# Performance work log

Hardware: AMD Instinct MI355X
Metric: run time of the kernel (lower is better)

The kernel has to match this reference:

```python
import jax, jax.numpy as jnp
import numpy as np

N_NODES = 50000
N_EDGES = 800000
DIM = 128
LN_EPS = 1e-5


def setup_inputs() -> dict:
    key = jax.random.key(0)
    k1, k2, k3, k4 = jax.random.split(key, 4)
    h = jax.random.normal(k1, (N_NODES, DIM), dtype=jnp.float32)
    edge_index = jax.random.randint(k2, (2, N_EDGES), 0, N_NODES, dtype=jnp.int64)
    W = jax.random.normal(k3, (DIM, DIM), dtype=jnp.float32) / np.sqrt(DIM)
    b = jnp.zeros((DIM,), dtype=jnp.float32)
    gamma = jnp.ones((DIM,), dtype=jnp.float32)
    beta = jnp.zeros((DIM,), dtype=jnp.float32)
    t = jnp.zeros((), dtype=jnp.float32)
    return {"t": t, "h": h, "edge_index": edge_index, "batch_size": N_NODES,
            "W": W, "b": b, "gamma": gamma, "beta": beta}


def _gcn_conv(h, edge_index, W, b):
    """PyG-style GCNConv: D^{-1/2} (A+I) D^{-1/2} (h W) + b."""
    N = h.shape[0]
    loops = jnp.arange(N, dtype=edge_index.dtype)
    src = jnp.concatenate([edge_index[0], loops])  # [E+N]
    dst = jnp.concatenate([edge_index[1], loops])  # [E+N]
    # degree (with self loops) on destination nodes
    deg = jax.ops.segment_sum(jnp.ones_like(dst, dtype=h.dtype), dst, num_segments=N)
    dinv = jnp.where(deg > 0, jax.lax.rsqrt(deg), 0.0)
    norm = dinv[src] * dinv[dst]                    # [E+N]
    xw = h @ W                                      # [N, D]
    msg = xw[src] * norm[:, None]                   # gather + scale, [E+N, D]
    agg = jax.ops.segment_sum(msg, dst, num_segments=N)  # scatter-add, [N, D]
    return agg + b


def reference(t, h, edge_index, batch_size, W, b, gamma, beta):
    if h.ndim == 1:
        h = h[None, :]
    dh = _gcn_conv(h, edge_index, W, b)
    # LayerNorm over feature dim, then tanh
    mean = jnp.mean(dh, axis=-1, keepdims=True)
    var = jnp.mean(jnp.square(dh - mean), axis=-1, keepdims=True)
    dh = (dh - mean) * jax.lax.rsqrt(var + LN_EPS) * gamma + beta
    dh = jnp.tanh(dh)
    return (dh, jnp.zeros_like(edge_index), jnp.zeros_like(jnp.asarray(batch_size)))
```

## Files before the change

### kernel.cpp

```cpp
#include <hip/hip_runtime.h>
#include <math.h>

#define NN 50000
#define NE 800000
#define D  128
#define SCAN_CHUNK 1024
#define NSCAN ((NN + SCAN_CHUNK - 1) / SCAN_CHUNK)
#define PG_BLOCKS 782

typedef __attribute__((ext_vector_type(8))) short bf16x8;
typedef __attribute__((ext_vector_type(4))) float f32x4;

__device__ __forceinline__ unsigned short f32_to_bf16(float f) {
    unsigned u = __float_as_uint(f);
    u = u + 0x7FFFu + ((u >> 16) & 1u);
    return (unsigned short)(u >> 16);
}

__global__ __launch_bounds__(256) void k_count(
        const float* __restrict__ Wg, const int* __restrict__ ei,
        int* __restrict__ deg, unsigned short* __restrict__ rank,
        unsigned short* __restrict__ wpk, unsigned short* __restrict__ zb,
        int* __restrict__ outtail, int tailN) {
    int tid = threadIdx.x;
    int g = blockIdx.x * 256 + tid;

    if (g < NE / 4) {
        int4 d4 = ((const int4*)(ei + NE))[g];
        ushort4 r;
        r.x = (unsigned short)atomicAdd(&deg[d4.x], 1);
        r.y = (unsigned short)atomicAdd(&deg[d4.y], 1);
        r.z = (unsigned short)atomicAdd(&deg[d4.z], 1);
        r.w = (unsigned short)atomicAdd(&deg[d4.w], 1);
        ((ushort4*)rank)[g] = r;
    }
    for (int i = g; i < tailN; i += PG_BLOCKS * 256) outtail[i] = 0;

    if (blockIdx.x == 0) {
#pragma unroll 8
        for (int i = 0; i < 64; i++) {
            int o = i * 256 + tid;
            int j = o & 7, frag = o >> 3;
            int lo = frag & 15, quad = (frag >> 4) & 3;
            int kt = (frag >> 6) & 3, nt = frag >> 8;
            int k = kt * 32 + quad * 8 + j, n = nt * 16 + lo;
            wpk[o] = f32_to_bf16(Wg[k * 128 + n]);
        }
    }
    if (blockIdx.x == 1 && tid < 64)
        ((unsigned*)(zb + (size_t)NN * D))[tid] = 0u;
}

__global__ __launch_bounds__(256) void k_scan(const int* __restrict__ deg,
                                              int* __restrict__ partial,
                                              int* __restrict__ flag,
                                              int* __restrict__ rowoff,
                                              float* __restrict__ dinv) {
    __shared__ int sbuf[256];
    int t = threadIdx.x;
    int bid = blockIdx.x;
    int base = bid * SCAN_CHUNK + t * 4;
    int d[4]; int s = 0;
#pragma unroll
    for (int j = 0; j < 4; j++) {
        int i = base + j;
        d[j] = 0;
        if (i < NN) {
            d[j] = deg[i];
            s += d[j];
            dinv[i] = rsqrtf((float)d[j] + 1.0f);
        }
    }
    sbuf[t] = s; __syncthreads();
    for (int off = 1; off < 256; off <<= 1) {
        int v = (t >= off) ? sbuf[t - off] : 0;
        __syncthreads();
        sbuf[t] += v;
        __syncthreads();
    }
    if (t == 0) {
        atomicExch(&partial[bid], sbuf[255]);
        __threadfence();
        atomicAdd(flag, 1);
        while (atomicAdd(flag, 0) < NSCAN) {}
    }
    __syncthreads();

    int lane = t & 63;
    int pv = (lane < NSCAN && lane < bid) ? atomicAdd(&partial[lane], 0) : 0;
#pragma unroll
    for (int off = 32; off > 0; off >>= 1) pv += __shfl_xor(pv, off, 64);

    int ex = sbuf[t] - s + pv;
#pragma unroll
    for (int j = 0; j < 4; j++) {
        int i = base + j;
        if (i < NN) {
            rowoff[i] = ex;
            ex += d[j];
            if (i == NN - 1) rowoff[NN] = ex;
        }
    }
}

__global__ __launch_bounds__(256) void k_gemm_fill(
        const float* __restrict__ h, const uint4* __restrict__ wpk4,
        const int* __restrict__ ei, const unsigned short* __restrict__ rank,
        const int* __restrict__ rowoff, const float* __restrict__ dinv,
        unsigned short* __restrict__ zb, int* __restrict__ csr) {
    int tid = threadIdx.x;
    int g = blockIdx.x * 256 + tid;

    if (g < NE / 4) {
        int4 s4 = ((const int4*)ei)[g];
        int4 d4 = ((const int4*)(ei + NE))[g];
        ushort4 r4 = ((const ushort4*)rank)[g];
        csr[rowoff[d4.x] + r4.x] = s4.x;
        csr[rowoff[d4.y] + r4.y] = s4.y;
        csr[rowoff[d4.z] + r4.z] = s4.z;
        csr[rowoff[d4.w] + r4.w] = s4.w;
    }

    int w = tid >> 6, lane = tid & 63;
    int quad = lane >> 4, lo = lane & 15;
    int rowBase = blockIdx.x * 64 + w * 16;
    int rowA = rowBase + lo; if (rowA > NN - 1) rowA = NN - 1;
    const float4* h4 = (const float4*)h;

    bf16x8 af[4];
#pragma unroll
    for (int kt = 0; kt < 4; kt++) {
        float4 u = h4[(size_t)rowA * 32 + kt * 8 + quad * 2];
        float4 v = h4[(size_t)rowA * 32 + kt * 8 + quad * 2 + 1];
        bf16x8 a;
        a[0] = (short)f32_to_bf16(u.x); a[1] = (short)f32_to_bf16(u.y);
        a[2] = (short)f32_to_bf16(u.z); a[3] = (short)f32_to_bf16(u.w);
        a[4] = (short)f32_to_bf16(v.x); a[5] = (short)f32_to_bf16(v.y);
        a[6] = (short)f32_to_bf16(v.z); a[7] = (short)f32_to_bf16(v.w);
        af[kt] = a;
    }

    f32x4 acc[8];
#pragma unroll
    for (int nt = 0; nt < 8; nt++) acc[nt] = (f32x4){0.f, 0.f, 0.f, 0.f};

#pragma unroll
    for (int kt = 0; kt < 4; kt++) {
#pragma unroll
        for (int nt = 0; nt < 8; nt++) {
            uint4 tb = wpk4[nt * 256 + kt * 64 + lane];
            bf16x8 bfv = __builtin_bit_cast(bf16x8, tb);
            acc[nt] = __builtin_amdgcn_mfma_f32_16x16x32_bf16(af[kt], bfv, acc[nt], 0, 0, 0);
        }
    }

#pragma unroll
    for (int reg = 0; reg < 4; reg++) {
        int row = rowBase + quad * 4 + reg;
        if (row < NN) {
            float dn = dinv[row];
#pragma unroll
            for (int nt = 0; nt < 8; nt++)
                zb[(size_t)row * D + nt * 16 + lo] = f32_to_bf16(acc[nt][reg] * dn);
        }
    }
}

__global__ __launch_bounds__(256) void k_gather_ln(
        const int* __restrict__ rowoff, const int* __restrict__ csr,
        const float* __restrict__ dinv, const unsigned* __restrict__ zbu,
        const float* __restrict__ bias, const float* __restrict__ gamma,
        const float* __restrict__ beta, float* __restrict__ out) {
    int tid = threadIdx.x;
    int w = tid >> 6, lane = tid & 63;
    int rowBase = blockIdx.x * 16 + w * 4;

    float2 x[4];
#pragma unroll
    for (int r = 0; r < 4; r++) {
        int row = __builtin_amdgcn_readfirstlane(rowBase + r);
        float dn = dinv[row];
        unsigned zr = zbu[(size_t)row * 64 + lane];
        float2 a;
        a.x = __uint_as_float(zr << 16);
        a.y = __uint_as_float(zr & 0xFFFF0000u);
        int cs = __builtin_amdgcn_readfirstlane(rowoff[row]);
        int ce = __builtin_amdgcn_readfirstlane(rowoff[row + 1]);
        for (int c = cs; c < ce; c += 8) {
            int m = ce - c;
            int s[8];
#pragma unroll
            for (int q = 0; q < 8; q++) {
                int t = csr[c + q];
                s[q] = (q < m) ? t : NN;
            }
            unsigned p[8];
#pragma unroll
            for (int q = 0; q < 8; q++)
                p[q] = zbu[(size_t)s[q] * 64 + lane];
#pragma unroll
            for (int q = 0; q < 8; q++) {
                a.x += __uint_as_float(p[q] << 16);
                a.y += __uint_as_float(p[q] & 0xFFFF0000u);
            }
        }
        a.x *= dn; a.y *= dn;
        x[r] = a;
    }

    float2 bi = ((const float2*)bias)[lane];
    float2 ga = ((const float2*)gamma)[lane];
    float2 be = ((const float2*)beta)[lane];
#pragma unroll
    for (int r = 0; r < 4; r++) {
        int row = rowBase + r;
        float y0 = x[r].x + bi.x;
        float y1 = x[r].y + bi.y;
        float s = y0 + y1;
#pragma unroll
        for (int off = 32; off > 0; off >>= 1) s += __shfl_xor(s, off, 64);
        float m = s * (1.0f / 128.0f);
        float v0 = y0 - m, v1 = y1 - m;
        float vs = v0 * v0 + v1 * v1;
#pragma unroll
        for (int off = 32; off > 0; off >>= 1) vs += __shfl_xor(vs, off, 64);
        float rstd = rsqrtf(vs * (1.0f / 128.0f) + 1e-5f);
        float2 o;
        o.x = tanhf(v0 * rstd * ga.x + be.x);
        o.y = tanhf(v1 * rstd * ga.y + be.y);
        *(float2*)&out[(size_t)row * D + lane * 2] = o;
    }
}

extern "C" void kernel_launch(void* const* d_in, const int* in_sizes, int n_in,
                              void* d_out, int out_size, void* d_ws, size_t ws_size,
                              hipStream_t stream) {
    const float* h     = (const float*)d_in[1];
    const int*   ei    = (const int*)  d_in[2];
    const float* Wg    = (const float*)d_in[4];
    const float* b     = (const float*)d_in[5];
    const float* gamma = (const float*)d_in[6];
    const float* beta  = (const float*)d_in[7];
    float* out = (float*)d_out;

    char* wsb = (char*)d_ws;
    unsigned short* wpk    = (unsigned short*)(wsb);
    int*            deg    = (int*)(wsb + 32768);
    int*            flag   = (int*)(wsb + 232768);
    int*            partial= (int*)(wsb + 232832);
    unsigned short* rank   = (unsigned short*)(wsb + 233088);
    int*            rowoff = (int*)(wsb + 1833088);
    float*          dinv   = (float*)(wsb + 2633152);
    int*            csr    = (int*)(wsb + 2833152);
    unsigned short* zb     = (unsigned short*)(wsb + 6033152);

    int tailN = out_size - NN * D;
    int* outtail = (int*)(out + (size_t)NN * D);

    hipMemsetAsync(deg, 0, NN * sizeof(int) + sizeof(int), stream);
    k_count    <<<PG_BLOCKS, 256, 0, stream>>>(Wg, ei, deg, rank, wpk, zb, outtail, tailN);
    k_scan     <<<NSCAN,     256, 0, stream>>>(deg, partial, flag, rowoff, dinv);
    k_gemm_fill<<<PG_BLOCKS, 256, 0, stream>>>(h, (const uint4*)wpk, ei, rank, rowoff, dinv, zb, csr);
    k_gather_ln<<<NN / 16,   256, 0, stream>>>(rowoff, csr, dinv, (const unsigned*)zb, b, gamma, beta, out);
}
```

Before: 196.1 us.

## Batch CSR index loads per wave, use wave-shuffle scan and fast tanh

The gather kernel now loads up to 64 neighbor indices per wave in one coalesced load and broadcasts them with readlane. It gathers 16 rows at a time instead of 8, and hoists the row offsets and self-loop loads for all four rows up front, to cut scalar index-load latency and raise memory-level parallelism. The scan kernel replaces the shared-memory Hillis-Steele loop with a wave shuffle scan plus per-wave sums, removing many barriers. tanhf is replaced by an exp/rcp approximation, which risks small accuracy loss and overflow for large inputs. The zb buffer offset is shifted so csr reads past the end stay in bounds.

```diff
diff --git a/kernel.cpp b/kernel.cpp
--- a/kernel.cpp
+++ b/kernel.cpp
@@ -15,6 +15,11 @@
     unsigned u = __float_as_uint(f);
     u = u + 0x7FFFu + ((u >> 16) & 1u);
     return (unsigned short)(u >> 16);
+}
+
+__device__ __forceinline__ float fast_tanh(float x) {
+    float e = __expf(2.0f * x);
+    return fmaf(-2.0f, __builtin_amdgcn_rcpf(e + 1.0f), 1.0f);
 }
 
 __global__ __launch_bounds__(256) void k_count(
@@ -56,9 +61,10 @@
                                               int* __restrict__ flag,
                                               int* __restrict__ rowoff,
                                               float* __restrict__ dinv) {
-    __shared__ int sbuf[256];
+    __shared__ int wsum[4];
     int t = threadIdx.x;
     int bid = blockIdx.x;
+    int lane = t & 63, wv = t >> 6;
     int base = bid * SCAN_CHUNK + t * 4;
     int d[4]; int s = 0;
 #pragma unroll
@@ -71,27 +77,32 @@
             dinv[i] = rsqrtf((float)d[j] + 1.0f);
         }
     }
-    sbuf[t] = s; __syncthreads();
-    for (int off = 1; off < 256; off <<= 1) {
-        int v = (t >= off) ? sbuf[t - off] : 0;
-        __syncthreads();
-        sbuf[t] += v;
-        __syncthreads();
-    }
-    if (t == 0) {
-        atomicExch(&partial[bid], sbuf[255]);
+    int v = s;
+#pragma unroll
+    for (int off = 1; off < 64; off <<= 1) {
+        int u = __shfl_up(v, off, 64);
+        if (lane >= off) v += u;
+    }
+    if (lane == 63) wsum[wv] = v;
+    __syncthreads();
+    int add = 0;
+#pragma unroll
+    for (int k = 0; k < 4; k++) if (k < wv) add += wsum[k];
+    int inc = v + add;
+
+    if (t == 255) {
+        atomicExch(&partial[bid], inc);
         __threadfence();
         atomicAdd(flag, 1);
         while (atomicAdd(flag, 0) < NSCAN) {}
     }
     __syncthreads();
 
-    int lane = t & 63;
     int pv = (lane < NSCAN && lane < bid) ? atomicAdd(&partial[lane], 0) : 0;
 #pragma unroll
     for (int off = 32; off > 0; off >>= 1) pv += __shfl_xor(pv, off, 64);
 
-    int ex = sbuf[t] - s + pv;
+    int ex = inc - s + pv;
 #pragma unroll
     for (int j = 0; j < 4; j++) {
         int i = base + j;
@@ -175,37 +186,54 @@
     int w = tid >> 6, lane = tid & 63;
     int rowBase = blockIdx.x * 16 + w * 4;
 
+    int cs[4], ce[4]; float dn[4]; unsigned selfz[4]; int v0[4];
+#pragma unroll
+    for (int r = 0; r < 4; r++) {
+        int row = rowBase + r;
+        cs[r] = __builtin_amdgcn_readfirstlane(rowoff[row]);
+        ce[r] = __builtin_amdgcn_readfirstlane(rowoff[row + 1]);
+        dn[r] = dinv[row];
+        selfz[r] = zbu[(size_t)row * 64 + lane];
+    }
+#pragma unroll
+    for (int r = 0; r < 4; r++) {
+        int m0 = ce[r] - cs[r]; if (m0 > 64) m0 = 64;
+        int t0 = csr[cs[r] + lane];
+        v0[r] = (lane < m0) ? t0 : NN;
+    }
+
     float2 x[4];
 #pragma unroll
     for (int r = 0; r < 4; r++) {
-        int row = __builtin_amdgcn_readfirstlane(rowBase + r);
-        float dn = dinv[row];
-        unsigned zr = zbu[(size_t)row * 64 + lane];
-        float2 a;
-        a.x = __uint_as_float(zr << 16);
-        a.y = __uint_as_float(zr & 0xFFFF0000u);
-        int cs = __builtin_amdgcn_readfirstlane(rowoff[row]);
-        int ce = __builtin_amdgcn_readfirstlane(rowoff[row + 1]);
-        for (int c = cs; c < ce; c += 8) {
-            int m = ce - c;
-            int s[8];
-#pragma unroll
-            for (int q = 0; q < 8; q++) {
-                int t = csr[c + q];
-                s[q] = (q < m) ? t : NN;
+        float ax = __uint_as_float(selfz[r] << 16);
+        float ay = __uint_as_float(selfz[r] & 0xFFFF0000u);
+        int c = cs[r];
+        int v = v0[r];
+        while (true) {
+            int m = ce[r] - c; if (m > 64) m = 64;
+            int nb = (m + 15) >> 4;
+            for (int jb = 0; jb < nb; ++jb) {
+                int j = jb << 4;
+                unsigned p[16];
+#pragma unroll
+                for (int q = 0; q < 16; q++) {
+                    int sq = __builtin_amdgcn_readlane(v, j + q);
+                    p[q] = zbu[(size_t)sq * 64 + lane];
+                }
+#pragma unroll
+                for (int q = 0; q < 16; q++) {
+                    ax += __uint_as_float(p[q] << 16);
+                    ay += __uint_as_float(p[q] & 0xFFFF0000u);
+                }
             }
-            unsigned p[8];
-#pragma unroll
-            for (int q = 0; q < 8; q++)
-                p[q] = zbu[(size_t)s[q] * 64 + lane];
-#pragma unroll
-            for (int q = 0; q < 8; q++) {
-                a.x += __uint_as_float(p[q] << 16);
-                a.y += __uint_as_float(p[q] & 0xFFFF0000u);
-            }
-        }
-        a.x *= dn; a.y *= dn;
-        x[r] = a;
+            c += 64;
+            if (c >= ce[r]) break;
+            int m2 = ce[r] - c; if (m2 > 64) m2 = 64;
+            int t2 = csr[c + lane];
+            v = (lane < m2) ? t2 : NN;
+        }
+        x[r].x = ax * dn[r];
+        x[r].y = ay * dn[r];
     }
 
     float2 bi = ((const float2*)bias)[lane];
@@ -220,14 +248,14 @@
 #pragma unroll
         for (int off = 32; off > 0; off >>= 1) s += __shfl_xor(s, off, 64);
         float m = s * (1.0f / 128.0f);
-        float v0 = y0 - m, v1 = y1 - m;
-        float vs = v0 * v0 + v1 * v1;
+        float v0f = y0 - m, v1f = y1 - m;
+        float vs = v0f * v0f + v1f * v1f;
 #pragma unroll
         for (int off = 32; off > 0; off >>= 1) vs += __shfl_xor(vs, off, 64);
         float rstd = rsqrtf(vs * (1.0f / 128.0f) + 1e-5f);
         float2 o;
-        o.x = tanhf(v0 * rstd * ga.x + be.x);
-        o.y = tanhf(v1 * rstd * ga.y + be.y);
+        o.x = fast_tanh(v0f * rstd * ga.x + be.x);
+        o.y = fast_tanh(v1f * rstd * ga.y + be.y);
         *(float2*)&out[(size_t)row * D + lane * 2] = o;
     }
 }
@@ -252,7 +280,7 @@
     int*            rowoff = (int*)(wsb + 1833088);
     float*          dinv   = (float*)(wsb + 2633152);
     int*            csr    = (int*)(wsb + 2833152);
-    unsigned short* zb     = (unsigned short*)(wsb + 6033152);
+    unsigned short* zb     = (unsigned short*)(wsb + 6033408);
 
     int tailN = out_size - NN * D;
     int* outtail = (int*)(out + (size_t)NN * D);
```

Result: slower. 202.5 us (+3.3%).
